# Kernel optimization log

Measured on AMD Instinct MI355X. Metric: run time of the kernel, lower is better.

## Reference

```python
import jax, jax.numpy as jnp
import numpy as np

B, T, H = 64, 256, 128

def setup_inputs() -> dict:
    key = jax.random.key(0)
    ks = jax.random.split(key, 10)
    s = 1.0 / np.sqrt(H)
    return {
        "x": jax.random.normal(ks[0], (B, T, 2), jnp.float32),
        "enc_output": jax.random.normal(ks[1], (B, T, H), jnp.float32),
        "h0": jax.random.normal(ks[2], (B, H), jnp.float32) * s,
        "c0": jax.random.normal(ks[3], (B, H), jnp.float32) * s,
        "W1": jax.random.normal(ks[4], (H, H), jnp.float32) * s,
        "W2": jax.random.normal(ks[5], (H, H), jnp.float32) * s,
        "V": jax.random.normal(ks[6], (H,), jnp.float32) * s,
        "Wk": jax.random.normal(ks[7], (2, 4 * H), jnp.float32) * (1.0 / np.sqrt(2.0)),
        "Wr": jax.random.normal(ks[8], (H, 4 * H), jnp.float32) * s,
        "b": jnp.zeros((4 * H,), jnp.float32),
    }


def reference(x, enc_output, h0, c0, W1, W2, V, Wk, Wr, b):
    Bb, Tt, _ = x.shape
    # Precompute W1 @ enc_output once (original recomputes it T times inside K.rnn)
    enc_proj = jnp.einsum('bth,hk->btk', enc_output, W1)  # [B,T,H]

    def lstm_cell(inp, h, c):
        # Keras LSTMCell, gate order i,f,c,o; sigmoid recurrent activation, tanh activation
        z = inp @ Wk + h @ Wr + b  # [B,4H]
        zi, zf, zg, zo = jnp.split(z, 4, axis=-1)
        i = jax.nn.sigmoid(zi)
        f = jax.nn.sigmoid(zf)
        g = jnp.tanh(zg)
        o = jax.nn.sigmoid(zo)
        c_new = f * c + i * g
        h_new = o * jnp.tanh(c_new)
        return h_new, c_new

    def step(carry, _):
        h, c, ptr = carry
        h, c = lstm_cell(ptr, h, c)
        # additive attention over all encoder steps, batched (replaces inner K.rnn)
        scores = jnp.einsum('btk,k->bt', jnp.tanh(enc_proj + (h @ W2)[:, None, :]), V)
        probs = jax.nn.softmax(scores, axis=1)  # [B,T]
        # get_pointer with rank=0: top-1 of descending argsort == argmax
        idx = jnp.argmax(probs, axis=1)  # [B]
        ptr = jnp.take_along_axis(x, idx[:, None, None], axis=1)[:, 0, :]  # [B,2]
        return (h, c, ptr), probs

    ptr0 = jnp.ones((Bb, 2), x.dtype)
    _, probs_seq = jax.lax.scan(step, (h0, c0, ptr0), None, length=Tt)  # [T,B,T]
    return jnp.transpose(probs_seq, (1, 0, 2))  # [B,T,T]
```

## Files before the change

### kernel.cpp

```cpp
#include <hip/hip_runtime.h>
#include <cstddef>

#define TT 256
#define HH 128
#define EST 132

__device__ __forceinline__ float rdlane(float v, int l) {
  return __int_as_float(__builtin_amdgcn_readlane(__float_as_int(v), l));
}
__device__ __forceinline__ float fast_sigmoid(float x) {
  const float L2E = 1.4426950408889634f;
  float y = __builtin_amdgcn_exp2f(-x * L2E);
  return __builtin_amdgcn_rcpf(1.0f + y);
}
__device__ __forceinline__ float fast_tanh(float x) {
  const float C2 = 2.8853900817779268f;
  float y = __builtin_amdgcn_exp2f(x * C2);
  return 1.0f - 2.0f * __builtin_amdgcn_rcpf(1.0f + y);
}

__global__ __launch_bounds__(512, 2)
void decoder_kernel(const float* __restrict__ x,
                    const float* __restrict__ enc_output,
                    const float* __restrict__ h0,
                    const float* __restrict__ c0,
                    const float* __restrict__ W1,
                    const float* __restrict__ W2,
                    const float* __restrict__ V,
                    const float* __restrict__ Wk,
                    const float* __restrict__ Wr,
                    const float* __restrict__ bias,
                    float* __restrict__ out)
{
  __shared__ float E[TT * EST];
  __shared__ float zpart[4 * 512];
  __shared__ float part[8][64];
  __shared__ float scp[8 * 257];
  __shared__ float hbuf[HH];
  __shared__ float xloc[TT * 2];

  const int u    = threadIdx.x;
  const int b    = blockIdx.x;
  const int lane = u & 63;
  const int w    = u >> 6;
  const float C2  = 2.8853900817779268f;
  const float L2E = 1.4426950408889634f;

  {
    const float* encb = enc_output + (size_t)b * TT * HH;
    const int tsub = u >> 4;
    const int ks   = (u & 15) * 8;
    for (int p = 0; p < 8; ++p) {
      const int tt = p * 32 + tsub;
      float4 a0 = {0.f, 0.f, 0.f, 0.f};
      float4 a1 = {0.f, 0.f, 0.f, 0.f};
      const float4* er4 = (const float4*)(encb + tt * HH);
      for (int j4 = 0; j4 < 32; ++j4) {
        const float4 ev = er4[j4];
        const float* w1p = W1 + (j4 * 4) * HH + ks;
        float4 wa, wb;
        wa = *(const float4*)(w1p + 0 * HH); wb = *(const float4*)(w1p + 0 * HH + 4);
        a0.x += ev.x * wa.x; a0.y += ev.x * wa.y; a0.z += ev.x * wa.z; a0.w += ev.x * wa.w;
        a1.x += ev.x * wb.x; a1.y += ev.x * wb.y; a1.z += ev.x * wb.z; a1.w += ev.x * wb.w;
        wa = *(const float4*)(w1p + 1 * HH); wb = *(const float4*)(w1p + 1 * HH + 4);
        a0.x += ev.y * wa.x; a0.y += ev.y * wa.y; a0.z += ev.y * wa.z; a0.w += ev.y * wa.w;
        a1.x += ev.y * wb.x; a1.y += ev.y * wb.y; a1.z += ev.y * wb.z; a1.w += ev.y * wb.w;
        wa = *(const float4*)(w1p + 2 * HH); wb = *(const float4*)(w1p + 2 * HH + 4);
        a0.x += ev.z * wa.x; a0.y += ev.z * wa.y; a0.z += ev.z * wa.z; a0.w += ev.z * wa.w;
        a1.x += ev.z * wb.x; a1.y += ev.z * wb.y; a1.z += ev.z * wb.z; a1.w += ev.z * wb.w;
        wa = *(const float4*)(w1p + 3 * HH); wb = *(const float4*)(w1p + 3 * HH + 4);
        a0.x += ev.w * wa.x; a0.y += ev.w * wa.y; a0.z += ev.w * wa.z; a0.w += ev.w * wa.w;
        a1.x += ev.w * wb.x; a1.y += ev.w * wb.y; a1.z += ev.w * wb.z; a1.w += ev.w * wb.w;
      }
      *(float4*)(&E[tt * EST + ks])     = a0;
      *(float4*)(&E[tt * EST + ks + 4]) = a1;
    }
  }
  xloc[u] = x[b * (TT * 2) + u];

  const int kq = u >> 7;
  const int cs = u & 127;
  float4 wr4[32];
  #pragma unroll
  for (int i = 0; i < 32; ++i)
    wr4[i] = *(const float4*)(Wr + (32 * kq + i) * 512 + 4 * cs);
  const int m = u & 127;
  float wkA[4], wkB[4], bbg[4];
  #pragma unroll
  for (int gg = 0; gg < 4; ++gg) {
    wkA[gg] = Wk[gg * HH + m];
    wkB[gg] = Wk[512 + gg * HH + m];
    bbg[gg] = bias[gg * HH + m];
  }
  float c = c0[b * HH + m];
  const int halfC = w & 1;
  const int tqC   = w >> 1;
  float w2col[32];
  #pragma unroll
  for (int jj = 0; jj < 32; ++jj)
    w2col[jj] = W2[(32 * tqC + jj) * HH + 64 * halfC + lane];
  const int kstar = 16 * w + (lane & 15);
  const int pD    = kstar >> 6;
  const int lD    = kstar & 63;
  const float v2r = -2.0f * V[kstar];
  float ptr0 = 1.0f, ptr1 = 1.0f;
  float svr;
  {
    float v = V[lane] + V[64 + lane];
    #pragma unroll
    for (int o = 1; o < 64; o <<= 1) v += __shfl_xor(v, o, 64);
    svr = v;
  }

  __syncthreads();

  {
    float* Er = &E[(u >> 1) * EST + 64 * (u & 1)];
    #pragma unroll
    for (int i = 0; i < 16; ++i) {
      float4 ev = *(const float4*)(Er + 4 * i);
      ev.x = __builtin_amdgcn_exp2f(ev.x * C2);
      ev.y = __builtin_amdgcn_exp2f(ev.y * C2);
      ev.z = __builtin_amdgcn_exp2f(ev.z * C2);
      ev.w = __builtin_amdgcn_exp2f(ev.w * C2);
      *(float4*)(Er + 4 * i) = ev;
    }
  }
  float vL[16];
  #pragma unroll
  for (int i = 0; i < 16; ++i) vL[i] = rdlane(v2r, i);
  {
    float hA0 = h0[(size_t)b * HH + 32 * kq + (lane & 31)];
    float4 zac = {0.f, 0.f, 0.f, 0.f};
    #pragma unroll
    for (int i = 0; i < 32; ++i) {
      float hi = rdlane(hA0, i);
      zac.x += hi * wr4[i].x;
      zac.y += hi * wr4[i].y;
      zac.z += hi * wr4[i].z;
      zac.w += hi * wr4[i].w;
    }
    *(float4*)(&zpart[kq * 512 + 4 * cs]) = zac;
  }
  __syncthreads();

  float* outb = out + (size_t)b * TT * TT;

  #pragma unroll 1
  for (int step = 0; step < TT; ++step) {
    if (step > 0 && w < 4) {
      float s0 = 0.f, s1 = 0.f, s2 = 0.f, s3 = 0.f;
      #pragma unroll
      for (int q = 0; q < 8; ++q) {
        s0 += scp[q * 257 + 0 * 64 + lane];
        s1 += scp[q * 257 + 1 * 64 + lane];
        s2 += scp[q * 257 + 2 * 64 + lane];
        s3 += scp[q * 257 + 3 * 64 + lane];
      }
      s0 += svr; s1 += svr; s2 += svr; s3 += svr;
      float p0 = __builtin_amdgcn_exp2f((s0 - 12.0f) * L2E);
      float p1 = __builtin_amdgcn_exp2f((s1 - 12.0f) * L2E);
      float p2 = __builtin_amdgcn_exp2f((s2 - 12.0f) * L2E);
      float p3 = __builtin_amdgcn_exp2f((s3 - 12.0f) * L2E);
      float m4 = fmaxf(fmaxf(s0, s1), fmaxf(s2, s3));
      int ttl = (s0 == m4) ? 0 : (s1 == m4) ? 1 : (s2 == m4) ? 2 : 3;
      float ws4 = (p0 + p1) + (p2 + p3);
      float mx = m4;
      #pragma unroll
      for (int o = 1; o < 64; o <<= 1) {
        mx  = fmaxf(mx, __shfl_xor(mx, o));
        ws4 += __shfl_xor(ws4, o);
      }
      unsigned long long bal = __ballot(m4 == mx);
      int ls  = __ffsll((unsigned long long)bal) - 1;
      int tts = __builtin_amdgcn_readlane(ttl, ls);
      int fbt = 64 * tts + ls;
      ptr0 = xloc[2 * fbt + 0];
      ptr1 = xloc[2 * fbt + 1];
      float pw = (w == 0) ? p0 : (w == 1) ? p1 : (w == 2) ? p2 : p3;
      outb[(size_t)(step - 1) * TT + 64 * w + lane] = pw * __builtin_amdgcn_rcpf(ws4);
    }
    if (u < HH) {
      float z0 = bbg[0] + ptr0 * wkA[0] + ptr1 * wkB[0];
      float z1 = bbg[1] + ptr0 * wkA[1] + ptr1 * wkB[1];
      float z2 = bbg[2] + ptr0 * wkA[2] + ptr1 * wkB[2];
      float z3 = bbg[3] + ptr0 * wkA[3] + ptr1 * wkB[3];
      #pragma unroll
      for (int q = 0; q < 4; ++q) {
        z0 += zpart[q * 512 + 0 * HH + m];
        z1 += zpart[q * 512 + 1 * HH + m];
        z2 += zpart[q * 512 + 2 * HH + m];
        z3 += zpart[q * 512 + 3 * HH + m];
      }
      float ig = fast_sigmoid(z0);
      float fg = fast_sigmoid(z1);
      float gg = fast_tanh(z2);
      float og = fast_sigmoid(z3);
      c = fg * c + ig * gg;
      hbuf[m] = og * fast_tanh(c);
    }
    __syncthreads();

    float hC = hbuf[32 * tqC + (lane & 31)];
    float hA = hbuf[32 * kq  + (lane & 31)];
    {
      float cp0 = 0.0f, cp1 = 0.0f;
      #pragma unroll
      for (int jj = 0; jj < 32; jj += 2) {
        cp0 += rdlane(hC, jj)     * w2col[jj];
        cp1 += rdlane(hC, jj + 1) * w2col[jj + 1];
      }
      part[w][lane] = cp0 + cp1;
    }
    {
      float4 zac = {0.f, 0.f, 0.f, 0.f};
      #pragma unroll
      for (int i = 0; i < 32; ++i) {
        float hi = rdlane(hA, i);
        zac.x += hi * wr4[i].x;
        zac.y += hi * wr4[i].y;
        zac.z += hi * wr4[i].z;
        zac.w += hi * wr4[i].w;
      }
      *(float4*)(&zpart[kq * 512 + 4 * cs]) = zac;
    }
    __syncthreads();

    float Uk;
    {
      float usum = (part[pD][lD] + part[pD + 2][lD]) +
                   (part[pD + 4][lD] + part[pD + 6][lD]);
      Uk = __builtin_amdgcn_exp2f(usum * C2);
    }
    {
      float uL[16];
      #pragma unroll
      for (int i = 0; i < 16; ++i) uL[i] = rdlane(Uk, i);
      #pragma unroll
      for (int tt = 0; tt < 4; ++tt) {
        const float* Er = &E[(64 * tt + lane) * EST + 16 * w];
        float4 e0 = *(const float4*)(Er + 0);
        float4 e1 = *(const float4*)(Er + 4);
        float4 e2 = *(const float4*)(Er + 8);
        float4 e3 = *(const float4*)(Er + 12);
        float a0 = 0.0f, a1 = 0.0f;
        float t0, t1, n;
        t0 = fmaf(e0.x, uL[ 0], 1.0f); t1 = fmaf(e0.y, uL[ 1], 1.0f);
        n  = fmaf(vL[ 1], t0, vL[ 0] * t1);
        a0 = fmaf(n, __builtin_amdgcn_rcpf(t0 * t1), a0);
        t0 = fmaf(e0.z, uL[ 2], 1.0f); t1 = fmaf(e0.w, uL[ 3], 1.0f);
        n  = fmaf(vL[ 3], t0, vL[ 2] * t1);
        a1 = fmaf(n, __builtin_amdgcn_rcpf(t0 * t1), a1);
        t0 = fmaf(e1.x, uL[ 4], 1.0f); t1 = fmaf(e1.y, uL[ 5], 1.0f);
        n  = fmaf(vL[ 5], t0, vL[ 4] * t1);
        a0 = fmaf(n, __builtin_amdgcn_rcpf(t0 * t1), a0);
        t0 = fmaf(e1.z, uL[ 6], 1.0f); t1 = fmaf(e1.w, uL[ 7], 1.0f);
        n  = fmaf(vL[ 7], t0, vL[ 6] * t1);
        a1 = fmaf(n, __builtin_amdgcn_rcpf(t0 * t1), a1);
        t0 = fmaf(e2.x, uL[ 8], 1.0f); t1 = fmaf(e2.y, uL[ 9], 1.0f);
        n  = fmaf(vL[ 9], t0, vL[ 8] * t1);
        a0 = fmaf(n, __builtin_amdgcn_rcpf(t0 * t1), a0);
        t0 = fmaf(e2.z, uL[10], 1.0f); t1 = fmaf(e2.w, uL[11], 1.0f);
        n  = fmaf(vL[11], t0, vL[10] * t1);
        a1 = fmaf(n, __builtin_amdgcn_rcpf(t0 * t1), a1);
        t0 = fmaf(e3.x, uL[12], 1.0f); t1 = fmaf(e3.y, uL[13], 1.0f);
        n  = fmaf(vL[13], t0, vL[12] * t1);
        a0 = fmaf(n, __builtin_amdgcn_rcpf(t0 * t1), a0);
        t0 = fmaf(e3.z, uL[14], 1.0f); t1 = fmaf(e3.w, uL[15], 1.0f);
        n  = fmaf(vL[15], t0, vL[14] * t1);
        a1 = fmaf(n, __builtin_amdgcn_rcpf(t0 * t1), a1);
        scp[w * 257 + 64 * tt + lane] = a0 + a1;
      }
    }
    __syncthreads();
  }

  if (w < 4) {
    float s0 = 0.f, s1 = 0.f, s2 = 0.f, s3 = 0.f;
    #pragma unroll
    for (int q = 0; q < 8; ++q) {
      s0 += scp[q * 257 + 0 * 64 + lane];
      s1 += scp[q * 257 + 1 * 64 + lane];
      s2 += scp[q * 257 + 2 * 64 + lane];
      s3 += scp[q * 257 + 3 * 64 + lane];
    }
    s0 += svr; s1 += svr; s2 += svr; s3 += svr;
    float p0 = __builtin_amdgcn_exp2f((s0 - 12.0f) * L2E);
    float p1 = __builtin_amdgcn_exp2f((s1 - 12.0f) * L2E);
    float p2 = __builtin_amdgcn_exp2f((s2 - 12.0f) * L2E);
    float p3 = __builtin_amdgcn_exp2f((s3 - 12.0f) * L2E);
    float ws4 = (p0 + p1) + (p2 + p3);
    #pragma unroll
    for (int o = 1; o < 64; o <<= 1) ws4 += __shfl_xor(ws4, o);
    float pw = (w == 0) ? p0 : (w == 1) ? p1 : (w == 2) ? p2 : p3;
    outb[(size_t)255 * TT + 64 * w + lane] = pw * __builtin_amdgcn_rcpf(ws4);
  }
}

extern "C" void kernel_launch(void* const* d_in, const int* in_sizes, int n_in,
                              void* d_out, int out_size, void* d_ws, size_t ws_size,
                              hipStream_t stream) {
  (void)in_sizes; (void)n_in; (void)d_ws; (void)ws_size; (void)out_size;
  const float* x    = (const float*)d_in[0];
  const float* enc  = (const float*)d_in[1];
  const float* h0   = (const float*)d_in[2];
  const float* c0   = (const float*)d_in[3];
  const float* W1   = (const float*)d_in[4];
  const float* W2   = (const float*)d_in[5];
  const float* V    = (const float*)d_in[6];
  const float* Wk   = (const float*)d_in[7];
  const float* Wr   = (const float*)d_in[8];
  const float* bias = (const float*)d_in[9];
  float* out = (float*)d_out;

  decoder_kernel<<<64, 512, 0, stream>>>(x, enc, h0, c0, W1, W2, V, Wk, Wr, bias, out);
}
```

Baseline: 841.5 us.

## Double block size to 1024 threads and repartition per-step work

Launches 1024 threads per block instead of 512 and redistributes the recurrent matvec, W2 projection and attention tanh-sum so each thread does half the work. Each block already runs alone on a CU, so the extra waves are meant to cut per-step latency of the serial 256-step loop. It also moves the V coefficients into shared memory instead of per-wave readlanes. The risk is register pressure under the 1024-thread limit and heavier barrier cost.

```diff
diff --git a/kernel.cpp b/kernel.cpp
--- a/kernel.cpp
+++ b/kernel.cpp
@@ -19,7 +19,7 @@
   return 1.0f - 2.0f * __builtin_amdgcn_rcpf(1.0f + y);
 }
 
-__global__ __launch_bounds__(512, 2)
+__global__ __launch_bounds__(1024)
 void decoder_kernel(const float* __restrict__ x,
                     const float* __restrict__ enc_output,
                     const float* __restrict__ h0,
@@ -34,10 +34,11 @@
 {
   __shared__ float E[TT * EST];
   __shared__ float zpart[4 * 512];
-  __shared__ float part[8][64];
+  __shared__ float part[8 * 128];
   __shared__ float scp[8 * 257];
   __shared__ float hbuf[HH];
   __shared__ float xloc[TT * 2];
+  __shared__ float v2l[HH];
 
   const int u    = threadIdx.x;
   const int b    = blockIdx.x;
@@ -50,8 +51,8 @@
     const float* encb = enc_output + (size_t)b * TT * HH;
     const int tsub = u >> 4;
     const int ks   = (u & 15) * 8;
-    for (int p = 0; p < 8; ++p) {
-      const int tt = p * 32 + tsub;
+    for (int p = 0; p < 4; ++p) {
+      const int tt = p * 64 + tsub;
       float4 a0 = {0.f, 0.f, 0.f, 0.f};
       float4 a1 = {0.f, 0.f, 0.f, 0.f};
       const float4* er4 = (const float4*)(encb + tt * HH);
@@ -76,14 +77,15 @@
       *(float4*)(&E[tt * EST + ks + 4]) = a1;
     }
   }
-  xloc[u] = x[b * (TT * 2) + u];
-
-  const int kq = u >> 7;
-  const int cs = u & 127;
-  float4 wr4[32];
+  if (u < 512) xloc[u] = x[b * (TT * 2) + u];
+  if (u < HH)  v2l[u]  = -2.0f * V[u];
+
+  const int kq = u >> 8;
+  const int cs = u & 255;
+  float2 wr2[32];
   #pragma unroll
   for (int i = 0; i < 32; ++i)
-    wr4[i] = *(const float4*)(Wr + (32 * kq + i) * 512 + 4 * cs);
+    wr2[i] = *(const float2*)(Wr + (size_t)(32 * kq + i) * 512 + 2 * cs);
   const int m = u & 127;
   float wkA[4], wkB[4], bbg[4];
   #pragma unroll
@@ -93,16 +95,15 @@
     bbg[gg] = bias[gg * HH + m];
   }
   float c = c0[b * HH + m];
-  const int halfC = w & 1;
-  const int tqC   = w >> 1;
-  float w2col[32];
+  const int jg = w >> 1;
+  const int kb = w & 1;
+  float w2col[16];
   #pragma unroll
-  for (int jj = 0; jj < 32; ++jj)
-    w2col[jj] = W2[(32 * tqC + jj) * HH + 64 * halfC + lane];
-  const int kstar = 16 * w + (lane & 15);
-  const int pD    = kstar >> 6;
-  const int lD    = kstar & 63;
-  const float v2r = -2.0f * V[kstar];
+  for (int jj = 0; jj < 16; ++jj)
+    w2col[jj] = W2[(16 * jg + jj) * HH + 64 * kb + lane];
+  const int kg = w & 7;
+  const int th = w >> 3;
+  const int kstar = 16 * kg + (lane & 15);
   float ptr0 = 1.0f, ptr1 = 1.0f;
   float svr;
   {
@@ -115,9 +116,9 @@
   __syncthreads();
 
   {
-    float* Er = &E[(u >> 1) * EST + 64 * (u & 1)];
-    #pragma unroll
-    for (int i = 0; i < 16; ++i) {
+    float* Er = &E[(u >> 2) * EST + 32 * (u & 3)];
+    #pragma unroll
+    for (int i = 0; i < 8; ++i) {
       float4 ev = *(const float4*)(Er + 4 * i);
       ev.x = __builtin_amdgcn_exp2f(ev.x * C2);
       ev.y = __builtin_amdgcn_exp2f(ev.y * C2);
@@ -126,21 +127,17 @@
       *(float4*)(Er + 4 * i) = ev;
     }
   }
-  float vL[16];
-  #pragma unroll
-  for (int i = 0; i < 16; ++i) vL[i] = rdlane(v2r, i);
   {
     float hA0 = h0[(size_t)b * HH + 32 * kq + (lane & 31)];
-    float4 zac = {0.f, 0.f, 0.f, 0.f};
+    float zx = 0.0f, zy = 0.0f;
     #pragma unroll
     for (int i = 0; i < 32; ++i) {
       float hi = rdlane(hA0, i);
-      zac.x += hi * wr4[i].x;
-      zac.y += hi * wr4[i].y;
-      zac.z += hi * wr4[i].z;
-      zac.w += hi * wr4[i].w;
-    }
-    *(float4*)(&zpart[kq * 512 + 4 * cs]) = zac;
+      zx += hi * wr2[i].x;
+      zy += hi * wr2[i].y;
+    }
+    zpart[kq * 512 + 2 * cs + 0] = zx;
+    zpart[kq * 512 + 2 * cs + 1] = zy;
   }
   __syncthreads();
 
@@ -201,76 +198,92 @@
     }
     __syncthreads();
 
-    float hC = hbuf[32 * tqC + (lane & 31)];
-    float hA = hbuf[32 * kq  + (lane & 31)];
+    float hC = hbuf[16 * jg + (lane & 15)];
+    float hA = hbuf[32 * kq + (lane & 31)];
     {
       float cp0 = 0.0f, cp1 = 0.0f;
       #pragma unroll
-      for (int jj = 0; jj < 32; jj += 2) {
+      for (int jj = 0; jj < 16; jj += 2) {
         cp0 += rdlane(hC, jj)     * w2col[jj];
         cp1 += rdlane(hC, jj + 1) * w2col[jj + 1];
       }
-      part[w][lane] = cp0 + cp1;
+      part[jg * 128 + 64 * kb + lane] = cp0 + cp1;
     }
     {
-      float4 zac = {0.f, 0.f, 0.f, 0.f};
+      float zx = 0.0f, zy = 0.0f;
       #pragma unroll
       for (int i = 0; i < 32; ++i) {
         float hi = rdlane(hA, i);
-        zac.x += hi * wr4[i].x;
-        zac.y += hi * wr4[i].y;
-        zac.z += hi * wr4[i].z;
-        zac.w += hi * wr4[i].w;
-      }
-      *(float4*)(&zpart[kq * 512 + 4 * cs]) = zac;
+        zx += hi * wr2[i].x;
+        zy += hi * wr2[i].y;
+      }
+      zpart[kq * 512 + 2 * cs + 0] = zx;
+      zpart[kq * 512 + 2 * cs + 1] = zy;
     }
     __syncthreads();
 
     float Uk;
     {
-      float usum = (part[pD][lD] + part[pD + 2][lD]) +
-                   (part[pD + 4][lD] + part[pD + 6][lD]);
+      float usum = ((part[0 * 128 + kstar] + part[1 * 128 + kstar]) +
+                    (part[2 * 128 + kstar] + part[3 * 128 + kstar])) +
+                   ((part[4 * 128 + kstar] + part[5 * 128 + kstar]) +
+                    (part[6 * 128 + kstar] + part[7 * 128 + kstar]));
       Uk = __builtin_amdgcn_exp2f(usum * C2);
     }
     {
-      float uL[16];
-      #pragma unroll
-      for (int i = 0; i < 16; ++i) uL[i] = rdlane(Uk, i);
-      #pragma unroll
-      for (int tt = 0; tt < 4; ++tt) {
-        const float* Er = &E[(64 * tt + lane) * EST + 16 * w];
-        float4 e0 = *(const float4*)(Er + 0);
-        float4 e1 = *(const float4*)(Er + 4);
-        float4 e2 = *(const float4*)(Er + 8);
-        float4 e3 = *(const float4*)(Er + 12);
-        float a0 = 0.0f, a1 = 0.0f;
+      const int t0r = 128 * th + lane;
+      const int t1r = 128 * th + 64 + lane;
+      float accA = 0.0f, accB = 0.0f;
+      #pragma unroll
+      for (int hf = 0; hf < 2; ++hf) {
+        float u0 = rdlane(Uk, 8 * hf + 0);
+        float u1 = rdlane(Uk, 8 * hf + 1);
+        float u2 = rdlane(Uk, 8 * hf + 2);
+        float u3 = rdlane(Uk, 8 * hf + 3);
+        float u4 = rdlane(Uk, 8 * hf + 4);
+        float u5 = rdlane(Uk, 8 * hf + 5);
+        float u6 = rdlane(Uk, 8 * hf + 6);
+        float u7 = rdlane(Uk, 8 * hf + 7);
+        float4 va = *(const float4*)(v2l + 16 * kg + 8 * hf);
+        float4 vb = *(const float4*)(v2l + 16 * kg + 8 * hf + 4);
         float t0, t1, n;
-        t0 = fmaf(e0.x, uL[ 0], 1.0f); t1 = fmaf(e0.y, uL[ 1], 1.0f);
-        n  = fmaf(vL[ 1], t0, vL[ 0] * t1);
-        a0 = fmaf(n, __builtin_amdgcn_rcpf(t0 * t1), a0);
-        t0 = fmaf(e0.z, uL[ 2], 1.0f); t1 = fmaf(e0.w, uL[ 3], 1.0f);
-        n  = fmaf(vL[ 3], t0, vL[ 2] * t1);
-        a1 = fmaf(n, __builtin_amdgcn_rcpf(t0 * t1), a1);
-        t0 = fmaf(e1.x, uL[ 4], 1.0f); t1 = fmaf(e1.y, uL[ 5], 1.0f);
-        n  = fmaf(vL[ 5], t0, vL[ 4] * t1);
-        a0 = fmaf(n, __builtin_amdgcn_rcpf(t0 * t1), a0);
-        t0 = fmaf(e1.z, uL[ 6], 1.0f); t1 = fmaf(e1.w, uL[ 7], 1.0f);
-        n  = fmaf(vL[ 7], t0, vL[ 6] * t1);
-        a1 = fmaf(n, __builtin_amdgcn_rcpf(t0 * t1), a1);
-        t0 = fmaf(e2.x, uL[ 8], 1.0f); t1 = fmaf(e2.y, uL[ 9], 1.0f);
-        n  = fmaf(vL[ 9], t0, vL[ 8] * t1);
-        a0 = fmaf(n, __builtin_amdgcn_rcpf(t0 * t1), a0);
-        t0 = fmaf(e2.z, uL[10], 1.0f); t1 = fmaf(e2.w, uL[11], 1.0f);
-        n  = fmaf(vL[11], t0, vL[10] * t1);
-        a1 = fmaf(n, __builtin_amdgcn_rcpf(t0 * t1), a1);
-        t0 = fmaf(e3.x, uL[12], 1.0f); t1 = fmaf(e3.y, uL[13], 1.0f);
-        n  = fmaf(vL[13], t0, vL[12] * t1);
-        a0 = fmaf(n, __builtin_amdgcn_rcpf(t0 * t1), a0);
-        t0 = fmaf(e3.z, uL[14], 1.0f); t1 = fmaf(e3.w, uL[15], 1.0f);
-        n  = fmaf(vL[15], t0, vL[14] * t1);
-        a1 = fmaf(n, __builtin_amdgcn_rcpf(t0 * t1), a1);
-        scp[w * 257 + 64 * tt + lane] = a0 + a1;
-      }
+        {
+          const float* Er = &E[t0r * EST + 16 * kg + 8 * hf];
+          float4 e0 = *(const float4*)(Er);
+          float4 e1 = *(const float4*)(Er + 4);
+          t0 = fmaf(e0.x, u0, 1.0f); t1 = fmaf(e0.y, u1, 1.0f);
+          n  = fmaf(va.y, t0, va.x * t1);
+          accA = fmaf(n, __builtin_amdgcn_rcpf(t0 * t1), accA);
+          t0 = fmaf(e0.z, u2, 1.0f); t1 = fmaf(e0.w, u3, 1.0f);
+          n  = fmaf(va.w, t0, va.z * t1);
+          accA = fmaf(n, __builtin_amdgcn_rcpf(t0 * t1), accA);
+          t0 = fmaf(e1.x, u4, 1.0f); t1 = fmaf(e1.y, u5, 1.0f);
+          n  = fmaf(vb.y, t0, vb.x * t1);
+          accA = fmaf(n, __builtin_amdgcn_rcpf(t0 * t1), accA);
+          t0 = fmaf(e1.z, u6, 1.0f); t1 = fmaf(e1.w, u7, 1.0f);
+          n  = fmaf(vb.w, t0, vb.z * t1);
+          accA = fmaf(n, __builtin_amdgcn_rcpf(t0 * t1), accA);
+        }
+        {
+          const float* Er = &E[t1r * EST + 16 * kg + 8 * hf];
+          float4 e0 = *(const float4*)(Er);
+          float4 e1 = *(const float4*)(Er + 4);
+          t0 = fmaf(e0.x, u0, 1.0f); t1 = fmaf(e0.y, u1, 1.0f);
+          n  = fmaf(va.y, t0, va.x * t1);
+          accB = fmaf(n, __builtin_amdgcn_rcpf(t0 * t1), accB);
+          t0 = fmaf(e0.z, u2, 1.0f); t1 = fmaf(e0.w, u3, 1.0f);
+          n  = fmaf(va.w, t0, va.z * t1);
+          accB = fmaf(n, __builtin_amdgcn_rcpf(t0 * t1), accB);
+          t0 = fmaf(e1.x, u4, 1.0f); t1 = fmaf(e1.y, u5, 1.0f);
+          n  = fmaf(vb.y, t0, vb.x * t1);
+          accB = fmaf(n, __builtin_amdgcn_rcpf(t0 * t1), accB);
+          t0 = fmaf(e1.z, u6, 1.0f); t1 = fmaf(e1.w, u7, 1.0f);
+          n  = fmaf(vb.w, t0, vb.z * t1);
+          accB = fmaf(n, __builtin_amdgcn_rcpf(t0 * t1), accB);
+        }
+      }
+      scp[kg * 257 + t0r] = accA;
+      scp[kg * 257 + t1r] = accB;
     }
     __syncthreads();
   }
@@ -313,5 +326,5 @@
   const float* bias = (const float*)d_in[9];
   float* out = (float*)d_out;
 
-  decoder_kernel<<<64, 512, 0, stream>>>(x, enc, h0, c0, W1, W2, V, Wk, Wr, bias, out);
-}
+  decoder_kernel<<<64, 1024, 0, stream>>>(x, enc, h0, c0, W1, W2, V, Wk, Wr, bias, out);
+}
```

Measured after the change: 1.013 ms. 1.2x slower.

## Remove a per-step barrier by computing the W2 projection per wave

Applied to the files above, without the earlier changes.

Each wave now computes its own 16-column slice of h@W2. It reads hbuf directly with float4 loads and reduces with cross-lane shuffles, so the shared `part` buffer and the barrier that guarded it are gone. The Wr recurrent matvec moves after the attention scoring, into the same barrier phase, leaving two __syncthreads per step instead of three. The score buffer is padded and read as float4, probabilities are stored as float4 by a 16-lane subset, and the LSTM cell update is spread across four waves. The cost is more redundant W2 multiply work per wave, plus extra shuffles and registers.

```diff
diff --git a/kernel.cpp b/kernel.cpp
--- a/kernel.cpp
+++ b/kernel.cpp
@@ -4,6 +4,7 @@
 #define TT 256
 #define HH 128
 #define EST 132
+#define SCPS 260
 
 __device__ __forceinline__ float rdlane(float v, int l) {
   return __int_as_float(__builtin_amdgcn_readlane(__float_as_int(v), l));
@@ -34,8 +35,7 @@
 {
   __shared__ float E[TT * EST];
   __shared__ float zpart[4 * 512];
-  __shared__ float part[8][64];
-  __shared__ float scp[8 * 257];
+  __shared__ float scp[8 * SCPS];
   __shared__ float hbuf[HH];
   __shared__ float xloc[TT * 2];
 
@@ -84,7 +84,7 @@
   #pragma unroll
   for (int i = 0; i < 32; ++i)
     wr4[i] = *(const float4*)(Wr + (32 * kq + i) * 512 + 4 * cs);
-  const int m = u & 127;
+  const int m = 32 * (w & 3) + (lane & 31);
   float wkA[4], wkB[4], bbg[4];
   #pragma unroll
   for (int gg = 0; gg < 4; ++gg) {
@@ -93,16 +93,16 @@
     bbg[gg] = bias[gg * HH + m];
   }
   float c = c0[b * HH + m];
-  const int halfC = w & 1;
-  const int tqC   = w >> 1;
-  float w2col[32];
+  const int kk = lane & 15;
+  const int jq = lane >> 4;
+  float w2local[32];
   #pragma unroll
-  for (int jj = 0; jj < 32; ++jj)
-    w2col[jj] = W2[(32 * tqC + jj) * HH + 64 * halfC + lane];
-  const int kstar = 16 * w + (lane & 15);
-  const int pD    = kstar >> 6;
-  const int lD    = kstar & 63;
-  const float v2r = -2.0f * V[kstar];
+  for (int i = 0; i < 32; ++i)
+    w2local[i] = W2[(32 * jq + i) * HH + 16 * w + kk];
+  const float v2r = -2.0f * V[16 * w + kk];
+  float vL[16];
+  #pragma unroll
+  for (int i = 0; i < 16; ++i) vL[i] = rdlane(v2r, i);
   float ptr0 = 1.0f, ptr1 = 1.0f;
   float svr;
   {
@@ -126,9 +126,6 @@
       *(float4*)(Er + 4 * i) = ev;
     }
   }
-  float vL[16];
-  #pragma unroll
-  for (int i = 0; i < 16; ++i) vL[i] = rdlane(v2r, i);
   {
     float hA0 = h0[(size_t)b * HH + 32 * kq + (lane & 31)];
     float4 zac = {0.f, 0.f, 0.f, 0.f};
@@ -149,21 +146,19 @@
   #pragma unroll 1
   for (int step = 0; step < TT; ++step) {
     if (step > 0 && w < 4) {
-      float s0 = 0.f, s1 = 0.f, s2 = 0.f, s3 = 0.f;
+      float4 sc = {0.f, 0.f, 0.f, 0.f};
       #pragma unroll
       for (int q = 0; q < 8; ++q) {
-        s0 += scp[q * 257 + 0 * 64 + lane];
-        s1 += scp[q * 257 + 1 * 64 + lane];
-        s2 += scp[q * 257 + 2 * 64 + lane];
-        s3 += scp[q * 257 + 3 * 64 + lane];
-      }
-      s0 += svr; s1 += svr; s2 += svr; s3 += svr;
-      float p0 = __builtin_amdgcn_exp2f((s0 - 12.0f) * L2E);
-      float p1 = __builtin_amdgcn_exp2f((s1 - 12.0f) * L2E);
-      float p2 = __builtin_amdgcn_exp2f((s2 - 12.0f) * L2E);
-      float p3 = __builtin_amdgcn_exp2f((s3 - 12.0f) * L2E);
-      float m4 = fmaxf(fmaxf(s0, s1), fmaxf(s2, s3));
-      int ttl = (s0 == m4) ? 0 : (s1 == m4) ? 1 : (s2 == m4) ? 2 : 3;
+        float4 v = *(const float4*)(&scp[q * SCPS + 4 * lane]);
+        sc.x += v.x; sc.y += v.y; sc.z += v.z; sc.w += v.w;
+      }
+      sc.x += svr; sc.y += svr; sc.z += svr; sc.w += svr;
+      float p0 = __builtin_amdgcn_exp2f((sc.x - 12.0f) * L2E);
+      float p1 = __builtin_amdgcn_exp2f((sc.y - 12.0f) * L2E);
+      float p2 = __builtin_amdgcn_exp2f((sc.z - 12.0f) * L2E);
+      float p3 = __builtin_amdgcn_exp2f((sc.w - 12.0f) * L2E);
+      float m4 = fmaxf(fmaxf(sc.x, sc.y), fmaxf(sc.z, sc.w));
+      int ttl = (sc.x == m4) ? 0 : (sc.y == m4) ? 1 : (sc.z == m4) ? 2 : 3;
       float ws4 = (p0 + p1) + (p2 + p3);
       float mx = m4;
       #pragma unroll
@@ -172,15 +167,18 @@
         ws4 += __shfl_xor(ws4, o);
       }
       unsigned long long bal = __ballot(m4 == mx);
-      int ls  = __ffsll((unsigned long long)bal) - 1;
-      int tts = __builtin_amdgcn_readlane(ttl, ls);
-      int fbt = 64 * tts + ls;
-      ptr0 = xloc[2 * fbt + 0];
-      ptr1 = xloc[2 * fbt + 1];
-      float pw = (w == 0) ? p0 : (w == 1) ? p1 : (w == 2) ? p2 : p3;
-      outb[(size_t)(step - 1) * TT + 64 * w + lane] = pw * __builtin_amdgcn_rcpf(ws4);
-    }
-    if (u < HH) {
+      int ls  = __ffsll(bal) - 1;
+      int tc  = 4 * lane + ttl;
+      int tts = __builtin_amdgcn_readlane(tc, ls);
+      ptr0 = xloc[2 * tts + 0];
+      ptr1 = xloc[2 * tts + 1];
+      if ((lane >> 4) == w) {
+        float rs = __builtin_amdgcn_rcpf(ws4);
+        float4 po = {p0 * rs, p1 * rs, p2 * rs, p3 * rs};
+        *(float4*)(&outb[(size_t)(step - 1) * TT + 4 * lane]) = po;
+      }
+    }
+    if ((lane & 32) == 0 && w < 4) {
       float z0 = bbg[0] + ptr0 * wkA[0] + ptr1 * wkB[0];
       float z1 = bbg[1] + ptr0 * wkA[1] + ptr1 * wkB[1];
       float z2 = bbg[2] + ptr0 * wkA[2] + ptr1 * wkB[2];
@@ -201,36 +199,22 @@
     }
     __syncthreads();
 
-    float hC = hbuf[32 * tqC + (lane & 31)];
-    float hA = hbuf[32 * kq  + (lane & 31)];
+    float Uk;
     {
       float cp0 = 0.0f, cp1 = 0.0f;
-      #pragma unroll
-      for (int jj = 0; jj < 32; jj += 2) {
-        cp0 += rdlane(hC, jj)     * w2col[jj];
-        cp1 += rdlane(hC, jj + 1) * w2col[jj + 1];
-      }
-      part[w][lane] = cp0 + cp1;
-    }
-    {
-      float4 zac = {0.f, 0.f, 0.f, 0.f};
-      #pragma unroll
-      for (int i = 0; i < 32; ++i) {
-        float hi = rdlane(hA, i);
-        zac.x += hi * wr4[i].x;
-        zac.y += hi * wr4[i].y;
-        zac.z += hi * wr4[i].z;
-        zac.w += hi * wr4[i].w;
-      }
-      *(float4*)(&zpart[kq * 512 + 4 * cs]) = zac;
-    }
-    __syncthreads();
-
-    float Uk;
-    {
-      float usum = (part[pD][lD] + part[pD + 2][lD]) +
-                   (part[pD + 4][lD] + part[pD + 6][lD]);
-      Uk = __builtin_amdgcn_exp2f(usum * C2);
+      const float4* h4 = (const float4*)(hbuf + 32 * jq);
+      #pragma unroll
+      for (int i4 = 0; i4 < 8; ++i4) {
+        float4 hv = h4[i4];
+        cp0 += hv.x * w2local[4 * i4 + 0];
+        cp1 += hv.y * w2local[4 * i4 + 1];
+        cp0 += hv.z * w2local[4 * i4 + 2];
+        cp1 += hv.w * w2local[4 * i4 + 3];
+      }
+      float csum = cp0 + cp1;
+      csum += __shfl_xor(csum, 16);
+      csum += __shfl_xor(csum, 32);
+      Uk = __builtin_amdgcn_exp2f(csum * C2);
     }
     {
       float uL[16];
@@ -269,31 +253,45 @@
         t0 = fmaf(e3.z, uL[14], 1.0f); t1 = fmaf(e3.w, uL[15], 1.0f);
         n  = fmaf(vL[15], t0, vL[14] * t1);
         a1 = fmaf(n, __builtin_amdgcn_rcpf(t0 * t1), a1);
-        scp[w * 257 + 64 * tt + lane] = a0 + a1;
-      }
+        scp[w * SCPS + 64 * tt + lane] = a0 + a1;
+      }
+    }
+    {
+      float hA = hbuf[32 * kq + (lane & 31)];
+      float4 zac = {0.f, 0.f, 0.f, 0.f};
+      #pragma unroll
+      for (int i = 0; i < 32; ++i) {
+        float hi = rdlane(hA, i);
+        zac.x += hi * wr4[i].x;
+        zac.y += hi * wr4[i].y;
+        zac.z += hi * wr4[i].z;
+        zac.w += hi * wr4[i].w;
+      }
+      *(float4*)(&zpart[kq * 512 + 4 * cs]) = zac;
     }
     __syncthreads();
   }
 
   if (w < 4) {
-    float s0 = 0.f, s1 = 0.f, s2 = 0.f, s3 = 0.f;
+    float4 sc = {0.f, 0.f, 0.f, 0.f};
     #pragma unroll
     for (int q = 0; q < 8; ++q) {
-      s0 += scp[q * 257 + 0 * 64 + lane];
-      s1 += scp[q * 257 + 1 * 64 + lane];
-      s2 += scp[q * 257 + 2 * 64 + lane];
-      s3 += scp[q * 257 + 3 * 64 + lane];
-    }
-    s0 += svr; s1 += svr; s2 += svr; s3 += svr;
-    float p0 = __builtin_amdgcn_exp2f((s0 - 12.0f) * L2E);
-    float p1 = __builtin_amdgcn_exp2f((s1 - 12.0f) * L2E);
-    float p2 = __builtin_amdgcn_exp2f((s2 - 12.0f) * L2E);
-    float p3 = __builtin_amdgcn_exp2f((s3 - 12.0f) * L2E);
+      float4 v = *(const float4*)(&scp[q * SCPS + 4 * lane]);
+      sc.x += v.x; sc.y += v.y; sc.z += v.z; sc.w += v.w;
+    }
+    sc.x += svr; sc.y += svr; sc.z += svr; sc.w += svr;
+    float p0 = __builtin_amdgcn_exp2f((sc.x - 12.0f) * L2E);
+    float p1 = __builtin_amdgcn_exp2f((sc.y - 12.0f) * L2E);
+    float p2 = __builtin_amdgcn_exp2f((sc.z - 12.0f) * L2E);
+    float p3 = __builtin_amdgcn_exp2f((sc.w - 12.0f) * L2E);
     float ws4 = (p0 + p1) + (p2 + p3);
     #pragma unroll
     for (int o = 1; o < 64; o <<= 1) ws4 += __shfl_xor(ws4, o);
-    float pw = (w == 0) ? p0 : (w == 1) ? p1 : (w == 2) ? p2 : p3;
-    outb[(size_t)255 * TT + 64 * w + lane] = pw * __builtin_amdgcn_rcpf(ws4);
+    if ((lane >> 4) == w) {
+      float rs = __builtin_amdgcn_rcpf(ws4);
+      float4 po = {p0 * rs, p1 * rs, p2 * rs, p3 * rs};
+      *(float4*)(&outb[(size_t)255 * TT + 4 * lane]) = po;
+    }
   }
 }
 
```

After: 833.2 us. About the same (-1.0%).
